# Kernel optimization log

Hardware: AMD Instinct MI355X
Metric: run time of the kernel (lower is better)

## Reference

```python
import jax, jax.numpy as jnp
import numpy as np

B, L, D, H, DFF = 8, 1024, 256, 8, 2048
DH = D // H


def setup_inputs() -> dict:
    key = jax.random.key(0)
    ks = jax.random.split(key, 12)

    def w(k, shape):
        return jax.random.normal(k, shape, dtype=jnp.float32) * 0.02

    # continuous padding: first `length` tokens valid, rest padded (mask True = pad)
    lengths = jax.random.randint(ks[0], (B,), L // 4, L + 1)
    mask = jnp.arange(L)[None, :] >= lengths[:, None]

    return {
        "src": jax.random.normal(ks[1], (B, L, D), dtype=jnp.float32),
        "src_key_padding_mask": mask,
        "in_proj_w": w(ks[2], (3 * D, D)),
        "in_proj_b": w(ks[3], (3 * D,)),
        "out_w": w(ks[4], (D, D)),
        "out_b": w(ks[5], (D,)),
        "proj_w": w(ks[6], (D, D)),
        "proj_b": w(ks[7], (D,)),
        "ff1_w": w(ks[8], (DFF, D)),
        "ff1_b": w(ks[9], (DFF,)),
        "ff2_w": w(ks[10], (D, DFF)),
        "ff2_b": w(ks[11], (D,)),
    }


def reference(src, src_key_padding_mask, in_proj_w, in_proj_b, out_w, out_b,
              proj_w, proj_b, ff1_w, ff1_b, ff2_w, ff2_b):
    mask = src_key_padding_mask  # [B, L], True = padding
    neg_inf = jnp.float32(-jnp.inf)

    # --- make_attn_mask (vectorized, continuous padding) ---
    s = (~mask).sum(axis=1).astype(jnp.float32)              # [B] valid lengths
    idx = jnp.arange(L, dtype=jnp.float32)
    dist = jnp.abs(idx[:, None] - idx[None, :])              # [L, L]
    valid_tok = idx[None, :] < s[:, None]                    # [B, L]
    pair_ok = valid_tok[:, :, None] & valid_tok[:, None, :]  # [B, L, L]
    bias = jnp.where(pair_ok, (s[:, None, None] - dist[None]) / s[:, None, None], neg_inf)
    # rows that are entirely -inf (padded query rows) are zeroed, like masked_fill
    row_pad = ~valid_tok                                     # [B, L]
    bias = jnp.where(row_pad[:, :, None], 0.0, bias)
    # key_padding_mask is merged additively (as in nn.MultiheadAttention)
    add_mask = bias + jnp.where(mask[:, None, :], neg_inf, 0.0)  # [B, L, L]

    # --- multi-head self-attention ---
    qkv = src @ in_proj_w.T + in_proj_b                      # [B, L, 3D]
    q, k, v = jnp.split(qkv, 3, axis=-1)

    def heads(t):
        return t.reshape(B, L, H, DH).transpose(0, 2, 1, 3)  # [B, H, L, DH]

    q, k, v = heads(q), heads(k), heads(v)
    scale = 1.0 / jnp.sqrt(jnp.float32(DH))
    scores = jnp.einsum('bhqd,bhkd->bhqk', q, k) * scale + add_mask[:, None]
    attn = jax.nn.softmax(scores, axis=-1)
    ctx = jnp.einsum('bhqk,bhkd->bhqd', attn, v)
    ctx = ctx.transpose(0, 2, 1, 3).reshape(B, L, D)
    h_attn = ctx @ out_w.T + out_b

    # --- residual proj + FFN (no layernorm, no dropout) ---
    h = src + (h_attn @ proj_w.T + proj_b)
    ff = jax.nn.gelu(h @ ff1_w.T + ff1_b, approximate=False) @ ff2_w.T + ff2_b
    h = h + ff

    # zero out padded rows (masked_fill with all_neg_inf)
    h = jnp.where(row_pad[:, :, None], 0.0, h)
    return h
```

## Files before the change

### kernel.cpp

```cpp
#include <hip/hip_runtime.h>
#include <hip/hip_bf16.h>


#define BB   8
#define LL   1024
#define DD   256
#define HHN  8
#define DHH  32
#define DFFN 2048

typedef __attribute__((ext_vector_type(8))) __bf16 bf16x8;
typedef __attribute__((ext_vector_type(4))) float f32x4;

__device__ inline void gload16(const void* g, void* l) {
  __builtin_amdgcn_global_load_lds(
      (const __attribute__((address_space(1))) void*)g,
      (__attribute__((address_space(3))) void*)l, 16, 0, 0);
}

__device__ inline bf16x8 cvt8(const float4 a, const float4 b) {
  bf16x8 o;
  o[0] = (__bf16)a.x; o[1] = (__bf16)a.y; o[2] = (__bf16)a.z; o[3] = (__bf16)a.w;
  o[4] = (__bf16)b.x; o[5] = (__bf16)b.y; o[6] = (__bf16)b.z; o[7] = (__bf16)b.w;
  return o;
}

#define NCVT2 (DFFN * DD)
#define NB_WC   128
#define NB_QKV  768
#define NB_CVT  512
#define BID_QKV  NB_WC
#define BID_CVT  (NB_WC + NB_QKV)
#define BID_LENS (BID_CVT + NB_CVT)
#define NB_TOTAL (BID_LENS + 1)

__global__ __launch_bounds__(256) void fused_pre_qkv(
    const float* __restrict__ src, const unsigned char* __restrict__ mb,
    const float* __restrict__ in_proj_w, const float* __restrict__ in_proj_b,
    const float* __restrict__ ff1_w, const float* __restrict__ ff2_w,
    const float* __restrict__ proj_w, const float* __restrict__ out_w,
    const float* __restrict__ proj_b, const float* __restrict__ out_b,
    __hip_bfloat16* __restrict__ qkv_bf, __hip_bfloat16* __restrict__ wff1_bf,
    __hip_bfloat16* __restrict__ wff2_bf, __hip_bfloat16* __restrict__ wc_bf,
    float* __restrict__ bc, int* __restrict__ lens) {
  __shared__ __bf16 As[2][64][32];
  __shared__ __bf16 Bs[2][128][32];
  __shared__ float red[256];
  __shared__ float pw[2][256];
  __shared__ int cnt8[BB];
  __shared__ int flag3f, flagNA;

  const int bid = blockIdx.x;
  const int tid = threadIdx.x;

  if (bid < NB_WC) {
    const int i0 = bid << 1;
    const int k = tid;
    pw[0][k] = proj_w[(size_t)i0 * DD + k];
    pw[1][k] = proj_w[(size_t)(i0 + 1) * DD + k];
    __syncthreads();
    float a0 = 0.f, a1 = 0.f;
#pragma unroll 8
    for (int n = 0; n < DD; ++n) {
      const float won = out_w[n * DD + k];
      a0 = fmaf(pw[0][n], won, a0);
      a1 = fmaf(pw[1][n], won, a1);
    }
    wc_bf[(size_t)i0 * DD + k] = (__hip_bfloat16)a0;
    wc_bf[(size_t)(i0 + 1) * DD + k] = (__hip_bfloat16)a1;
#pragma unroll
    for (int j = 0; j < 2; ++j) {
      red[k] = pw[j][k] * out_b[k];
      __syncthreads();
      for (int sft = 128; sft > 0; sft >>= 1) {
        if (k < sft) red[k] += red[k + sft];
        __syncthreads();
      }
      if (k == 0) bc[i0 + j] = proj_b[i0 + j] + red[0];
      __syncthreads();
    }
  } else if (bid < BID_CVT) {
    const int qb = bid - BID_QKV;
    const int x = qb % 6;
    const int y = qb / 6;
    const int c0 = x << 7;
    const int r0 = y << 6;
    const int w = tid >> 6;
    const int lane = tid & 63;
    const int c = lane & 15;
    const int hq = lane >> 4;
    const int h8 = hq << 3;
    const int wr = w >> 1, wc2 = w & 1;
    const int srow = tid >> 2;
    const int scol = (tid & 3) << 3;

    float4 ra[2], rb[2][2];
    auto LOADR = [&](int kt) {
      const int k0 = kt << 5;
      const float* ap = src + (size_t)(r0 + srow) * DD + k0 + scol;
      ra[0] = *(const float4*)ap;
      ra[1] = *(const float4*)(ap + 4);
#pragma unroll
      for (int ch = 0; ch < 2; ++ch) {
        const float* wp =
            in_proj_w + (size_t)(c0 + (ch << 6) + srow) * DD + k0 + scol;
        rb[ch][0] = *(const float4*)wp;
        rb[ch][1] = *(const float4*)(wp + 4);
      }
    };
    auto WRITEL = [&](int buf) {
      *(bf16x8*)&As[buf][srow][scol] = cvt8(ra[0], ra[1]);
#pragma unroll
      for (int ch = 0; ch < 2; ++ch)
        *(bf16x8*)&Bs[buf][(ch << 6) + srow][scol] = cvt8(rb[ch][0], rb[ch][1]);
    };

    f32x4 acc[2][4];
#pragma unroll
    for (int m = 0; m < 2; ++m)
#pragma unroll
      for (int n = 0; n < 4; ++n) acc[m][n] = (f32x4){0.f, 0.f, 0.f, 0.f};

    int buf = 0;
    LOADR(0);
    WRITEL(0);
    __syncthreads();
    for (int kt = 0; kt < 8; ++kt) {
      if (kt + 1 < 8) LOADR(kt + 1);
      bf16x8 af[2], bfr[4];
#pragma unroll
      for (int m = 0; m < 2; ++m)
        af[m] = *(const bf16x8*)&As[buf][wr * 32 + (m << 4) + c][h8];
#pragma unroll
      for (int n = 0; n < 4; ++n)
        bfr[n] = *(const bf16x8*)&Bs[buf][(wc2 << 6) + (n << 4) + c][h8];
#pragma unroll
      for (int m = 0; m < 2; ++m)
#pragma unroll
        for (int n = 0; n < 4; ++n)
          acc[m][n] = __builtin_amdgcn_mfma_f32_16x16x32_bf16(af[m], bfr[n],
                                                              acc[m][n], 0, 0, 0);
      if (kt + 1 < 8) WRITEL(buf ^ 1);
      __syncthreads();
      buf ^= 1;
    }

    float bv[4];
#pragma unroll
    for (int n = 0; n < 4; ++n)
      bv[n] = in_proj_b[c0 + (wc2 << 6) + (n << 4) + c];
#pragma unroll
    for (int m = 0; m < 2; ++m)
#pragma unroll
      for (int i = 0; i < 4; ++i) {
        const int gr = r0 + wr * 32 + (m << 4) + (hq << 2) + i;
#pragma unroll
        for (int n = 0; n < 4; ++n)
          qkv_bf[(size_t)gr * 768 + c0 + (wc2 << 6) + (n << 4) + c] =
              (__hip_bfloat16)(acc[m][n][i] + bv[n]);
      }
  } else if (bid < BID_LENS) {
    int i = (bid - BID_CVT) * 2048 + tid * 8;
    const float* s;
    __hip_bfloat16* d;
    if (i < NCVT2) { s = ff1_w; d = wff1_bf; }
    else { s = ff2_w; d = wff2_bf; i -= NCVT2; }
    const float4 a = *(const float4*)(s + i);
    const float4 b = *(const float4*)(s + i + 4);
    *(bf16x8*)(d + i) = cvt8(a, b);
  } else {
    if (tid == 0) { flag3f = 0; flagNA = 0; }
    if (tid < BB) cnt8[tid] = 0;
    __syncthreads();
    for (int i = tid; i < BB * LL; i += 256) {
      unsigned char v = mb[i];
      if (v) {
        if ((i & 3) == 3 && v == 0x3F) flag3f = 1;
        else if (i & 3) flagNA = 1;
      }
    }
    __syncthreads();
    const bool isfloat = (flag3f != 0);
    const bool isbool = (!isfloat) && (flagNA != 0);
    if (isbool) {
      for (int i = tid; i < BB * LL; i += 256)
        if (mb[i] == 0) atomicAdd(&cnt8[i >> 10], 1);
    } else {
      const int* mi = (const int*)mb;
      for (int i = tid; i < BB * LL; i += 256)
        if (mi[i] == 0) atomicAdd(&cnt8[i >> 10], 1);
    }
    __syncthreads();
    if (tid < BB) lens[tid] = cnt8[tid];
  }
}

template <int EPI, int BM, int BN>
__global__ __launch_bounds__(256) void gemm_bf16(
    const __hip_bfloat16* __restrict__ A, const __hip_bfloat16* __restrict__ W,
    const float* __restrict__ bias, const float* __restrict__ resid,
    float* __restrict__ Cf, __hip_bfloat16* __restrict__ Cb, const int M,
    const int N, const int K, const int* __restrict__ lens) {
  constexpr int MF = BM / 32;
  constexpr int NF = BN / 32;
  constexpr int CHA = BM / 64;
  constexpr int CHB = BN / 64;
  __shared__ __bf16 As[2][BM][32];
  __shared__ __bf16 Bs[2][BN][32];

  const int tid = threadIdx.x;
  const int w = tid >> 6;
  const int lane = tid & 63;
  const int c = lane & 15;
  const int hq = lane >> 4;
  const int h8 = hq << 3;
  const int wr = w >> 1, wc = w & 1;
  const int c0 = blockIdx.x * BN;
  const int r0 = blockIdx.y * BM;
  if ((r0 & (LL - 1)) >= lens[r0 >> 10]) return;

  const int srow = tid >> 2;
  const int scol = (tid & 3) << 3;

  auto STAGE = [&](int buf, int kt) {
    const int k0 = kt << 5;
#pragma unroll
    for (int ch = 0; ch < CHA; ++ch)
      gload16(A + (size_t)(r0 + (ch << 6) + srow) * K + k0 + scol,
              &As[buf][(ch << 6) + (w << 4)][0]);
#pragma unroll
    for (int ch = 0; ch < CHB; ++ch)
      gload16(W + (size_t)(c0 + (ch << 6) + srow) * K + k0 + scol,
              &Bs[buf][(ch << 6) + (w << 4)][0]);
  };

  f32x4 acc[MF][NF];
#pragma unroll
  for (int m = 0; m < MF; ++m)
#pragma unroll
    for (int n = 0; n < NF; ++n) acc[m][n] = (f32x4){0.f, 0.f, 0.f, 0.f};

  const int nkt = K >> 5;
  int buf = 0;
  STAGE(0, 0);
  __syncthreads();
  for (int kt = 0; kt < nkt; ++kt) {
    if (kt + 1 < nkt) STAGE(buf ^ 1, kt + 1);
    bf16x8 af[MF], bfr[NF];
#pragma unroll
    for (int m = 0; m < MF; ++m)
      af[m] = *(const bf16x8*)&As[buf][wr * (MF * 16) + (m << 4) + c][h8];
#pragma unroll
    for (int n = 0; n < NF; ++n)
      bfr[n] = *(const bf16x8*)&Bs[buf][wc * (NF * 16) + (n << 4) + c][h8];
#pragma unroll
    for (int m = 0; m < MF; ++m)
#pragma unroll
      for (int n = 0; n < NF; ++n)
        acc[m][n] =
            __builtin_amdgcn_mfma_f32_16x16x32_bf16(af[m], bfr[n], acc[m][n], 0, 0, 0);
    __syncthreads();
    buf ^= 1;
  }

  float bv[NF];
#pragma unroll
  for (int n = 0; n < NF; ++n) bv[n] = bias[c0 + wc * (NF * 16) + (n << 4) + c];

#pragma unroll
  for (int m = 0; m < MF; ++m) {
#pragma unroll
    for (int i = 0; i < 4; ++i) {
      const int gr = r0 + wr * (MF * 16) + (m << 4) + (hq << 2) + i;
#pragma unroll
      for (int n = 0; n < NF; ++n) {
        const int gc = c0 + wc * (NF * 16) + (n << 4) + c;
        float v = acc[m][n][i] + bv[n];
        if (EPI == 1) v = 0.5f * v * (1.0f + erff(v * 0.70710678118654752f));
        if (EPI == 2) {
          v += resid[(size_t)gr * N + gc];
          Cf[(size_t)gr * N + gc] = v;
        }
        Cb[(size_t)gr * N + gc] = (__hip_bfloat16)v;
      }
    }
  }
}

__global__ __launch_bounds__(256) void gemm_ff2_part(
    const __hip_bfloat16* __restrict__ A, const __hip_bfloat16* __restrict__ W,
    __hip_bfloat16* __restrict__ P, const int* __restrict__ lens) {
  __shared__ __bf16 As[2][64][32];
  __shared__ __bf16 Bs[2][128][32];

  const int tid = threadIdx.x;
  const int w = tid >> 6;
  const int lane = tid & 63;
  const int c = lane & 15;
  const int hq = lane >> 4;
  const int h8 = hq << 3;
  const int wr = w >> 1, wc = w & 1;
  const int c0 = blockIdx.x << 7;
  const int r0 = blockIdx.y << 6;
  if ((r0 & (LL - 1)) >= lens[r0 >> 10]) return;

  const int kz = blockIdx.z;
  const int kbase = kz << 9;
  const int srow = tid >> 2;
  const int scol = (tid & 3) << 3;

  auto STAGE = [&](int buf, int kt) {
    const int k0 = kbase + (kt << 5);
    gload16(A + (size_t)(r0 + srow) * DFFN + k0 + scol, &As[buf][w << 4][0]);
#pragma unroll
    for (int ch = 0; ch < 2; ++ch)
      gload16(W + (size_t)(c0 + (ch << 6) + srow) * DFFN + k0 + scol,
              &Bs[buf][(ch << 6) + (w << 4)][0]);
  };

  f32x4 acc[2][4];
#pragma unroll
  for (int m = 0; m < 2; ++m)
#pragma unroll
    for (int n = 0; n < 4; ++n) acc[m][n] = (f32x4){0.f, 0.f, 0.f, 0.f};

  int buf = 0;
  STAGE(0, 0);
  __syncthreads();
  for (int kt = 0; kt < 16; ++kt) {
    if (kt + 1 < 16) STAGE(buf ^ 1, kt + 1);
    bf16x8 af[2], bfr[4];
#pragma unroll
    for (int m = 0; m < 2; ++m)
      af[m] = *(const bf16x8*)&As[buf][wr * 32 + (m << 4) + c][h8];
#pragma unroll
    for (int n = 0; n < 4; ++n)
      bfr[n] = *(const bf16x8*)&Bs[buf][(wc << 6) + (n << 4) + c][h8];
#pragma unroll
    for (int m = 0; m < 2; ++m)
#pragma unroll
      for (int n = 0; n < 4; ++n)
        acc[m][n] =
            __builtin_amdgcn_mfma_f32_16x16x32_bf16(af[m], bfr[n], acc[m][n], 0, 0, 0);
    __syncthreads();
    buf ^= 1;
  }

  __hip_bfloat16* Pz = P + (size_t)kz * (BB * LL) * DD;
#pragma unroll
  for (int m = 0; m < 2; ++m)
#pragma unroll
    for (int i = 0; i < 4; ++i) {
      const int gr = r0 + wr * 32 + (m << 4) + (hq << 2) + i;
#pragma unroll
      for (int n = 0; n < 4; ++n)
        Pz[(size_t)gr * DD + c0 + (wc << 6) + (n << 4) + c] =
            (__hip_bfloat16)acc[m][n][i];
    }
}

__global__ __launch_bounds__(256) void ff2_reduce(
    const __hip_bfloat16* __restrict__ P, const float* __restrict__ resid,
    const float* __restrict__ bias, float* __restrict__ out,
    const int* __restrict__ lens) {
  const int idx = blockIdx.x * 256 + threadIdx.x;
  const int r = idx >> 6;
  const int c4 = (idx & 63) << 2;
  float4 o;
  if ((r & (LL - 1)) >= lens[r >> 10]) {
    o.x = o.y = o.z = o.w = 0.f;
  } else {
    const size_t base = (size_t)r * DD + c4;
    o = *(const float4*)&resid[base];
    const float4 bv = *(const float4*)&bias[c4];
    o.x += bv.x; o.y += bv.y; o.z += bv.z; o.w += bv.w;
#pragma unroll
    for (int z = 0; z < 4; ++z) {
      const ushort4 pu = *(const ushort4*)(P + (size_t)z * (BB * LL) * DD + base);
      o.x += __bfloat162float(*(const __hip_bfloat16*)&pu.x);
      o.y += __bfloat162float(*(const __hip_bfloat16*)&pu.y);
      o.z += __bfloat162float(*(const __hip_bfloat16*)&pu.z);
      o.w += __bfloat162float(*(const __hip_bfloat16*)&pu.w);
    }
  }
  *(float4*)&out[(size_t)r * DD + c4] = o;
}

__global__ __launch_bounds__(256) void attn_fwd_mfma(
    const __hip_bfloat16* __restrict__ qkv, __hip_bfloat16* __restrict__ ctx,
    const int* __restrict__ lens) {
  __shared__ __bf16 Ks[2][64][56];
  __shared__ __bf16 Vt[2][32][66];
  __shared__ __bf16 Pl[4][16][72];

  const int tid = threadIdx.x;
  const int q0 = blockIdx.x << 6;
  const int hh = blockIdx.y;
  const int b = blockIdx.z;
  const int slen = lens[b];
  if (q0 >= slen) return;

  const int w = tid >> 6;
  const int lane = tid & 63;
  const int c = lane & 15;
  const int h = lane >> 4;
  const int h8 = h << 3;

  const float L2E = 1.44269504f;
  const float sf = (float)slen;
  const float cb = -7.0f * L2E;
  const float cd = (1.0f / sf) * L2E;
  const float qscale = 0.17677669529663689f * L2E;

  bf16x8 qf;
  {
    const int qrow = q0 + (w << 4) + c;
    const bf16x8 qraw =
        *(const bf16x8*)(qkv + (size_t)(b * LL + qrow) * 768 + hh * DHH + h8);
#pragma unroll
    for (int j = 0; j < 8; ++j) qf[j] = (__bf16)((float)qraw[j] * qscale);
  }

  f32x4 acc0 = {0.f, 0.f, 0.f, 0.f};
  f32x4 acc1 = {0.f, 0.f, 0.f, 0.f};
  float lsum[4] = {0.f, 0.f, 0.f, 0.f};

  const int skey = tid >> 2;
  const int sdg = (tid & 3) << 3;
  const int ntk = (slen + 63) >> 6;
  const int qg = q0 + (w << 4) + (h << 2);

  const __hip_bfloat16* kvbase = qkv + (size_t)b * LL * 768 + 256 + hh * DHH + sdg;

  bf16x8 kreg, vreg;
  {
    const __hip_bfloat16* kb = kvbase + (size_t)skey * 768;
    kreg = *(const bf16x8*)kb;
    vreg = *(const bf16x8*)(kb + 256);
    *(bf16x8*)&Ks[0][skey][sdg] = kreg;
#pragma unroll
    for (int j = 0; j < 8; ++j) Vt[0][sdg + j][skey] = vreg[j];
  }
  if (ntk > 1) {
    const __hip_bfloat16* kb = kvbase + (size_t)(64 + skey) * 768;
    kreg = *(const bf16x8*)kb;
    vreg = *(const bf16x8*)(kb + 256);
  }
  __syncthreads();

  for (int kt = 0; kt < ntk; ++kt) {
    const int p = kt & 1;
    const int kbase = kt << 6;

    f32x4 st[4];
    __builtin_amdgcn_s_setprio(1);
#pragma unroll
    for (int t = 0; t < 4; ++t) {
      const bf16x8 kf = *(const bf16x8*)&Ks[p][(t << 4) + c][h8];
      st[t] = __builtin_amdgcn_mfma_f32_16x16x32_bf16(
          qf, kf, (f32x4){0.f, 0.f, 0.f, 0.f}, 0, 0, 0);
    }
    __builtin_amdgcn_s_setprio(0);

    if (kbase + 64 <= slen) {
#pragma unroll
      for (int t = 0; t < 4; ++t) {
        const float kjf = (float)(kbase + (t << 4) + c);
#pragma unroll
        for (int i = 0; i < 4; ++i) {
          const float dist = fabsf((float)(qg + i) - kjf);
          const float pv = __builtin_amdgcn_exp2f(st[t][i] + cb - dist * cd);
          lsum[i] += pv;
          Pl[w][(h << 2) + i][c + (t << 4)] = (__bf16)pv;
        }
      }
    } else {
#pragma unroll
      for (int t = 0; t < 4; ++t) {
        const int kj = kbase + (t << 4) + c;
        const bool kvalid = kj < slen;
        const float kjf = (float)kj;
#pragma unroll
        for (int i = 0; i < 4; ++i) {
          const float dist = fabsf((float)(qg + i) - kjf);
          const float arg = kvalid ? (st[t][i] + cb - dist * cd) : -1e30f;
          const float pv = __builtin_amdgcn_exp2f(arg);
          lsum[i] += pv;
          Pl[w][(h << 2) + i][c + (t << 4)] = (__bf16)pv;
        }
      }
    }

    asm volatile("s_waitcnt lgkmcnt(0)" ::: "memory");

    __builtin_amdgcn_s_setprio(1);
#pragma unroll
    for (int n = 0; n < 2; ++n) {
      const bf16x8 pf = *(const bf16x8*)&Pl[w][c][h8 + (n << 5)];
      const uint32_t* v0p = (const uint32_t*)&Vt[p][c][h8 + (n << 5)];
      const uint32_t* v1p = (const uint32_t*)&Vt[p][16 + c][h8 + (n << 5)];
      union { uint32_t u[4]; bf16x8 v; } t0, t1;
#pragma unroll
      for (int j = 0; j < 4; ++j) { t0.u[j] = v0p[j]; t1.u[j] = v1p[j]; }
      acc0 = __builtin_amdgcn_mfma_f32_16x16x32_bf16(pf, t0.v, acc0, 0, 0, 0);
      acc1 = __builtin_amdgcn_mfma_f32_16x16x32_bf16(pf, t1.v, acc1, 0, 0, 0);
    }
    __builtin_amdgcn_s_setprio(0);

    if (kt + 1 < ntk) {
      *(bf16x8*)&Ks[p ^ 1][skey][sdg] = kreg;
#pragma unroll
      for (int j = 0; j < 8; ++j) Vt[p ^ 1][sdg + j][skey] = vreg[j];
      if (kt + 2 < ntk) {
        const __hip_bfloat16* kb = kvbase + (size_t)(((kt + 2) << 6) + skey) * 768;
        kreg = *(const bf16x8*)kb;
        vreg = *(const bf16x8*)(kb + 256);
      }
    }
    __syncthreads();
  }

#pragma unroll
  for (int i = 0; i < 4; ++i) {
    float l = lsum[i];
    l += __shfl_xor(l, 1);
    l += __shfl_xor(l, 2);
    l += __shfl_xor(l, 4);
    l += __shfl_xor(l, 8);
    const float il = 1.0f / l;
    __hip_bfloat16* op =
        ctx + (size_t)(b * LL + q0 + (w << 4) + (h << 2) + i) * 256 + hh * DHH;
    op[c] = (__hip_bfloat16)(acc0[i] * il);
    op[c + 16] = (__hip_bfloat16)(acc1[i] * il);
  }
}

extern "C" void kernel_launch(void* const* d_in, const int* in_sizes, int n_in,
                              void* d_out, int out_size, void* d_ws,
                              size_t ws_size, hipStream_t stream) {
  (void)in_sizes; (void)n_in; (void)out_size; (void)ws_size;
  const float* src = (const float*)d_in[0];
  const unsigned char* mask = (const unsigned char*)d_in[1];
  const float* in_proj_w = (const float*)d_in[2];
  const float* in_proj_b = (const float*)d_in[3];
  const float* out_w = (const float*)d_in[4];
  const float* out_b = (const float*)d_in[5];
  const float* proj_w = (const float*)d_in[6];
  const float* proj_b = (const float*)d_in[7];
  const float* ff1_w = (const float*)d_in[8];
  const float* ff1_b = (const float*)d_in[9];
  const float* ff2_w = (const float*)d_in[10];
  const float* ff2_b = (const float*)d_in[11];
  float* out = (float*)d_out;

  const int M = BB * LL;
  char* p = (char*)d_ws;
  __hip_bfloat16* qkv_bf = (__hip_bfloat16*)p; p += (size_t)M * 768 * 2;
  __hip_bfloat16* ctx_bf = (__hip_bfloat16*)p; p += (size_t)M * 256 * 2;
  float* hbuf_f = (float*)p;                    p += (size_t)M * 256 * 4;
  __hip_bfloat16* hbuf_bf = (__hip_bfloat16*)p; p += (size_t)M * 256 * 2;
  __hip_bfloat16* ff1o_bf = (__hip_bfloat16*)p; p += (size_t)M * 2048 * 2;
  __hip_bfloat16* wff1_bf = (__hip_bfloat16*)p; p += (size_t)2048 * 256 * 2;
  __hip_bfloat16* wff2_bf = (__hip_bfloat16*)p; p += (size_t)256 * 2048 * 2;
  __hip_bfloat16* wc_bf = (__hip_bfloat16*)p;   p += (size_t)256 * 256 * 2;
  float* bc = (float*)p;                        p += 256 * 4;
  int* lens = (int*)p;                          p += 256;
  __hip_bfloat16* pbuf = (__hip_bfloat16*)p;    p += (size_t)4 * M * 256 * 2;

  fused_pre_qkv<<<NB_TOTAL, 256, 0, stream>>>(
      src, mask, in_proj_w, in_proj_b, ff1_w, ff2_w, proj_w, out_w, proj_b,
      out_b, qkv_bf, wff1_bf, wff2_bf, wc_bf, bc, lens);

  attn_fwd_mfma<<<dim3(LL / 64, HHN, BB), 256, 0, stream>>>(qkv_bf, ctx_bf, lens);

  gemm_bf16<2, 64, 64><<<dim3(4, 128), 256, 0, stream>>>(
      ctx_bf, wc_bf, bc, src, hbuf_f, hbuf_bf, M, 256, 256, lens);

  gemm_bf16<1, 128, 128><<<dim3(16, 64), 256, 0, stream>>>(
      hbuf_bf, wff1_bf, ff1_b, nullptr, nullptr, ff1o_bf, M, 2048, 256, lens);

  gemm_ff2_part<<<dim3(2, 128, 4), 256, 0, stream>>>(ff1o_bf, wff2_bf, pbuf, lens);

  ff2_reduce<<<M * 256 / 4 / 256, 256, 0, stream>>>(pbuf, hbuf_f, ff2_b, out, lens);
}
```

Before: 114.2 us.

## Replace GEMMs with small-tile full-K-slab kernel and drop FF2 split-K reduction

```diff
diff --git a/kernel.cpp b/kernel.cpp
--- a/kernel.cpp
+++ b/kernel.cpp
@@ -11,12 +11,6 @@
 
 typedef __attribute__((ext_vector_type(8))) __bf16 bf16x8;
 typedef __attribute__((ext_vector_type(4))) float f32x4;
-
-__device__ inline void gload16(const void* g, void* l) {
-  __builtin_amdgcn_global_load_lds(
-      (const __attribute__((address_space(1))) void*)g,
-      (__attribute__((address_space(3))) void*)l, 16, 0, 0);
-}
 
 __device__ inline bf16x8 cvt8(const float4 a, const float4 b) {
   bf16x8 o;
@@ -195,18 +189,14 @@
   }
 }
 
-template <int EPI, int BM, int BN>
-__global__ __launch_bounds__(256) void gemm_bf16(
+template <int EPI, int NIT>
+__global__ __launch_bounds__(256) void gemm_os(
     const __hip_bfloat16* __restrict__ A, const __hip_bfloat16* __restrict__ W,
     const float* __restrict__ bias, const float* __restrict__ resid,
-    float* __restrict__ Cf, __hip_bfloat16* __restrict__ Cb, const int M,
-    const int N, const int K, const int* __restrict__ lens) {
-  constexpr int MF = BM / 32;
-  constexpr int NF = BN / 32;
-  constexpr int CHA = BM / 64;
-  constexpr int CHB = BN / 64;
-  __shared__ __bf16 As[2][BM][32];
-  __shared__ __bf16 Bs[2][BN][32];
+    float* __restrict__ Cf, __hip_bfloat16* __restrict__ Cb, const int N,
+    const int* __restrict__ lens) {
+  __shared__ __bf16 Al[32][264];
+  __shared__ __bf16 Bl[64][264];
 
   const int tid = threadIdx.x;
   const int w = tid >> 6;
@@ -215,175 +205,83 @@
   const int hq = lane >> 4;
   const int h8 = hq << 3;
   const int wr = w >> 1, wc = w & 1;
-  const int c0 = blockIdx.x * BN;
-  const int r0 = blockIdx.y * BM;
-  if ((r0 & (LL - 1)) >= lens[r0 >> 10]) return;
-
-  const int srow = tid >> 2;
-  const int scol = (tid & 3) << 3;
-
-  auto STAGE = [&](int buf, int kt) {
-    const int k0 = kt << 5;
-#pragma unroll
-    for (int ch = 0; ch < CHA; ++ch)
-      gload16(A + (size_t)(r0 + (ch << 6) + srow) * K + k0 + scol,
-              &As[buf][(ch << 6) + (w << 4)][0]);
-#pragma unroll
-    for (int ch = 0; ch < CHB; ++ch)
-      gload16(W + (size_t)(c0 + (ch << 6) + srow) * K + k0 + scol,
-              &Bs[buf][(ch << 6) + (w << 4)][0]);
+  const int c0 = blockIdx.x << 6;
+  const int r0 = blockIdx.y << 5;
+  const int K = NIT * 256;
+  const int mylen = lens[r0 >> 10];
+
+  if ((r0 & (LL - 1)) >= mylen) {
+    if (EPI == 3) {
+      const int rr = tid >> 3;
+      const int cc = (tid & 7) << 3;
+      const float4 z = {0.f, 0.f, 0.f, 0.f};
+      *(float4*)&Cf[(size_t)(r0 + rr) * N + c0 + cc] = z;
+      *(float4*)&Cf[(size_t)(r0 + rr) * N + c0 + cc + 4] = z;
+    }
+    return;
+  }
+
+  const int ar = tid >> 3, asg = (tid & 7) << 5;
+  const int br = tid >> 2, bsg = (tid & 3) << 6;
+
+  bf16x8 ra[4], rb[8];
+  auto LOADR = [&](int t) {
+    const __hip_bfloat16* ap = A + (size_t)(r0 + ar) * K + t * 256 + asg;
+#pragma unroll
+    for (int j = 0; j < 4; ++j) ra[j] = *(const bf16x8*)(ap + j * 8);
+    const __hip_bfloat16* bp = W + (size_t)(c0 + br) * K + t * 256 + bsg;
+#pragma unroll
+    for (int j = 0; j < 8; ++j) rb[j] = *(const bf16x8*)(bp + j * 8);
   };
-
-  f32x4 acc[MF][NF];
-#pragma unroll
-  for (int m = 0; m < MF; ++m)
-#pragma unroll
-    for (int n = 0; n < NF; ++n) acc[m][n] = (f32x4){0.f, 0.f, 0.f, 0.f};
-
-  const int nkt = K >> 5;
-  int buf = 0;
-  STAGE(0, 0);
+  auto WRITEL = [&]() {
+#pragma unroll
+    for (int j = 0; j < 4; ++j) *(bf16x8*)&Al[ar][asg + j * 8] = ra[j];
+#pragma unroll
+    for (int j = 0; j < 8; ++j) *(bf16x8*)&Bl[br][bsg + j * 8] = rb[j];
+  };
+
+  f32x4 acc[2] = {{0.f, 0.f, 0.f, 0.f}, {0.f, 0.f, 0.f, 0.f}};
+
+  LOADR(0);
+  WRITEL();
   __syncthreads();
-  for (int kt = 0; kt < nkt; ++kt) {
-    if (kt + 1 < nkt) STAGE(buf ^ 1, kt + 1);
-    bf16x8 af[MF], bfr[NF];
-#pragma unroll
-    for (int m = 0; m < MF; ++m)
-      af[m] = *(const bf16x8*)&As[buf][wr * (MF * 16) + (m << 4) + c][h8];
-#pragma unroll
-    for (int n = 0; n < NF; ++n)
-      bfr[n] = *(const bf16x8*)&Bs[buf][wc * (NF * 16) + (n << 4) + c][h8];
-#pragma unroll
-    for (int m = 0; m < MF; ++m)
-#pragma unroll
-      for (int n = 0; n < NF; ++n)
-        acc[m][n] =
-            __builtin_amdgcn_mfma_f32_16x16x32_bf16(af[m], bfr[n], acc[m][n], 0, 0, 0);
-    __syncthreads();
-    buf ^= 1;
-  }
-
-  float bv[NF];
-#pragma unroll
-  for (int n = 0; n < NF; ++n) bv[n] = bias[c0 + wc * (NF * 16) + (n << 4) + c];
-
-#pragma unroll
-  for (int m = 0; m < MF; ++m) {
-#pragma unroll
-    for (int i = 0; i < 4; ++i) {
-      const int gr = r0 + wr * (MF * 16) + (m << 4) + (hq << 2) + i;
-#pragma unroll
-      for (int n = 0; n < NF; ++n) {
-        const int gc = c0 + wc * (NF * 16) + (n << 4) + c;
-        float v = acc[m][n][i] + bv[n];
-        if (EPI == 1) v = 0.5f * v * (1.0f + erff(v * 0.70710678118654752f));
-        if (EPI == 2) {
-          v += resid[(size_t)gr * N + gc];
-          Cf[(size_t)gr * N + gc] = v;
-        }
-        Cb[(size_t)gr * N + gc] = (__hip_bfloat16)v;
-      }
-    }
-  }
-}
-
-__global__ __launch_bounds__(256) void gemm_ff2_part(
-    const __hip_bfloat16* __restrict__ A, const __hip_bfloat16* __restrict__ W,
-    __hip_bfloat16* __restrict__ P, const int* __restrict__ lens) {
-  __shared__ __bf16 As[2][64][32];
-  __shared__ __bf16 Bs[2][128][32];
-
-  const int tid = threadIdx.x;
-  const int w = tid >> 6;
-  const int lane = tid & 63;
-  const int c = lane & 15;
-  const int hq = lane >> 4;
-  const int h8 = hq << 3;
-  const int wr = w >> 1, wc = w & 1;
-  const int c0 = blockIdx.x << 7;
-  const int r0 = blockIdx.y << 6;
-  if ((r0 & (LL - 1)) >= lens[r0 >> 10]) return;
-
-  const int kz = blockIdx.z;
-  const int kbase = kz << 9;
-  const int srow = tid >> 2;
-  const int scol = (tid & 3) << 3;
-
-  auto STAGE = [&](int buf, int kt) {
-    const int k0 = kbase + (kt << 5);
-    gload16(A + (size_t)(r0 + srow) * DFFN + k0 + scol, &As[buf][w << 4][0]);
-#pragma unroll
-    for (int ch = 0; ch < 2; ++ch)
-      gload16(W + (size_t)(c0 + (ch << 6) + srow) * DFFN + k0 + scol,
-              &Bs[buf][(ch << 6) + (w << 4)][0]);
-  };
-
-  f32x4 acc[2][4];
-#pragma unroll
-  for (int m = 0; m < 2; ++m)
-#pragma unroll
-    for (int n = 0; n < 4; ++n) acc[m][n] = (f32x4){0.f, 0.f, 0.f, 0.f};
-
-  int buf = 0;
-  STAGE(0, 0);
-  __syncthreads();
-  for (int kt = 0; kt < 16; ++kt) {
-    if (kt + 1 < 16) STAGE(buf ^ 1, kt + 1);
-    bf16x8 af[2], bfr[4];
-#pragma unroll
-    for (int m = 0; m < 2; ++m)
-      af[m] = *(const bf16x8*)&As[buf][wr * 32 + (m << 4) + c][h8];
-#pragma unroll
-    for (int n = 0; n < 4; ++n)
-      bfr[n] = *(const bf16x8*)&Bs[buf][(wc << 6) + (n << 4) + c][h8];
-#pragma unroll
-    for (int m = 0; m < 2; ++m)
-#pragma unroll
-      for (int n = 0; n < 4; ++n)
-        acc[m][n] =
-            __builtin_amdgcn_mfma_f32_16x16x32_bf16(af[m], bfr[n], acc[m][n], 0, 0, 0);
-    __syncthreads();
-    buf ^= 1;
-  }
-
-  __hip_bfloat16* Pz = P + (size_t)kz * (BB * LL) * DD;
-#pragma unroll
-  for (int m = 0; m < 2; ++m)
-#pragma unroll
-    for (int i = 0; i < 4; ++i) {
-      const int gr = r0 + wr * 32 + (m << 4) + (hq << 2) + i;
-#pragma unroll
-      for (int n = 0; n < 4; ++n)
-        Pz[(size_t)gr * DD + c0 + (wc << 6) + (n << 4) + c] =
-            (__hip_bfloat16)acc[m][n][i];
-    }
-}
-
-__global__ __launch_bounds__(256) void ff2_reduce(
-    const __hip_bfloat16* __restrict__ P, const float* __restrict__ resid,
-    const float* __restrict__ bias, float* __restrict__ out,
-    const int* __restrict__ lens) {
-  const int idx = blockIdx.x * 256 + threadIdx.x;
-  const int r = idx >> 6;
-  const int c4 = (idx & 63) << 2;
-  float4 o;
-  if ((r & (LL - 1)) >= lens[r >> 10]) {
-    o.x = o.y = o.z = o.w = 0.f;
-  } else {
-    const size_t base = (size_t)r * DD + c4;
-    o = *(const float4*)&resid[base];
-    const float4 bv = *(const float4*)&bias[c4];
-    o.x += bv.x; o.y += bv.y; o.z += bv.z; o.w += bv.w;
-#pragma unroll
-    for (int z = 0; z < 4; ++z) {
-      const ushort4 pu = *(const ushort4*)(P + (size_t)z * (BB * LL) * DD + base);
-      o.x += __bfloat162float(*(const __hip_bfloat16*)&pu.x);
-      o.y += __bfloat162float(*(const __hip_bfloat16*)&pu.y);
-      o.z += __bfloat162float(*(const __hip_bfloat16*)&pu.z);
-      o.w += __bfloat162float(*(const __hip_bfloat16*)&pu.w);
-    }
-  }
-  *(float4*)&out[(size_t)r * DD + c4] = o;
+  for (int t = 0; t < NIT; ++t) {
+    if (t + 1 < NIT) LOADR(t + 1);
+#pragma unroll
+    for (int k0 = 0; k0 < 8; ++k0) {
+      const bf16x8 af = *(const bf16x8*)&Al[wr * 16 + c][k0 * 32 + h8];
+#pragma unroll
+      for (int n = 0; n < 2; ++n) {
+        const bf16x8 bf = *(const bf16x8*)&Bl[wc * 32 + (n << 4) + c][k0 * 32 + h8];
+        acc[n] = __builtin_amdgcn_mfma_f32_16x16x32_bf16(af, bf, acc[n], 0, 0, 0);
+      }
+    }
+    if (t + 1 < NIT) {
+      __syncthreads();
+      WRITEL();
+      __syncthreads();
+    }
+  }
+
+  float bv[2];
+#pragma unroll
+  for (int n = 0; n < 2; ++n) bv[n] = bias[c0 + wc * 32 + (n << 4) + c];
+
+#pragma unroll
+  for (int i = 0; i < 4; ++i) {
+    const int gr = r0 + wr * 16 + (hq << 2) + i;
+    const bool zrow = (EPI == 3) && ((gr & (LL - 1)) >= mylen);
+#pragma unroll
+    for (int n = 0; n < 2; ++n) {
+      const int gc = c0 + wc * 32 + (n << 4) + c;
+      float v = acc[n][i] + bv[n];
+      if (EPI == 1) v = 0.5f * v * (1.0f + erff(v * 0.70710678118654752f));
+      if (EPI >= 2) v += resid[(size_t)gr * N + gc];
+      if (EPI == 3 && zrow) v = 0.f;
+      if (EPI >= 2) Cf[(size_t)gr * N + gc] = v;
+      if (EPI != 3) Cb[(size_t)gr * N + gc] = (__hip_bfloat16)v;
+    }
+  }
 }
 
 __global__ __launch_bounds__(256) void attn_fwd_mfma(
@@ -565,7 +463,6 @@
   __hip_bfloat16* wc_bf = (__hip_bfloat16*)p;   p += (size_t)256 * 256 * 2;
   float* bc = (float*)p;                        p += 256 * 4;
   int* lens = (int*)p;                          p += 256;
-  __hip_bfloat16* pbuf = (__hip_bfloat16*)p;    p += (size_t)4 * M * 256 * 2;
 
   fused_pre_qkv<<<NB_TOTAL, 256, 0, stream>>>(
       src, mask, in_proj_w, in_proj_b, ff1_w, ff2_w, proj_w, out_w, proj_b,
@@ -573,13 +470,12 @@
 
   attn_fwd_mfma<<<dim3(LL / 64, HHN, BB), 256, 0, stream>>>(qkv_bf, ctx_bf, lens);
 
-  gemm_bf16<2, 64, 64><<<dim3(4, 128), 256, 0, stream>>>(
-      ctx_bf, wc_bf, bc, src, hbuf_f, hbuf_bf, M, 256, 256, lens);
-
-  gemm_bf16<1, 128, 128><<<dim3(16, 64), 256, 0, stream>>>(
-      hbuf_bf, wff1_bf, ff1_b, nullptr, nullptr, ff1o_bf, M, 2048, 256, lens);
-
-  gemm_ff2_part<<<dim3(2, 128, 4), 256, 0, stream>>>(ff1o_bf, wff2_bf, pbuf, lens);
-
-  ff2_reduce<<<M * 256 / 4 / 256, 256, 0, stream>>>(pbuf, hbuf_f, ff2_b, out, lens);
+  gemm_os<2, 1><<<dim3(4, 256), 256, 0, stream>>>(
+      ctx_bf, wc_bf, bc, src, hbuf_f, hbuf_bf, DD, lens);
+
+  gemm_os<1, 1><<<dim3(32, 256), 256, 0, stream>>>(
+      hbuf_bf, wff1_bf, ff1_b, nullptr, nullptr, ff1o_bf, DFFN, lens);
+
+  gemm_os<3, 8><<<dim3(4, 256), 256, 0, stream>>>(
+      ff1o_bf, wff2_bf, ff2_b, hbuf_f, out, nullptr, DD, lens);
 }
```

Result: slower. 149.3 us (+30.7%).

## Replace split-K FF2 GEMM and reduce kernel with single fused-epilogue GEMM

Applied to the files above, without the earlier changes.

```diff
diff --git a/kernel.cpp b/kernel.cpp
--- a/kernel.cpp
+++ b/kernel.cpp
@@ -217,7 +217,22 @@
   const int wr = w >> 1, wc = w & 1;
   const int c0 = blockIdx.x * BN;
   const int r0 = blockIdx.y * BM;
-  if ((r0 & (LL - 1)) >= lens[r0 >> 10]) return;
+  const int mylen = lens[r0 >> 10];
+
+  if ((r0 & (LL - 1)) >= mylen) {
+    if (EPI == 3) {
+      constexpr int NF4 = BM * BN / 4 / 256;
+#pragma unroll
+      for (int k = 0; k < NF4; ++k) {
+        const int f4 = k * 256 + tid;
+        const int rr = f4 / (BN / 4);
+        const int cc = (f4 % (BN / 4)) << 2;
+        *(float4*)&Cf[(size_t)(r0 + rr) * N + c0 + cc] =
+            (float4){0.f, 0.f, 0.f, 0.f};
+      }
+    }
+    return;
+  }
 
   const int srow = tid >> 2;
   const int scol = (tid & 3) << 3;
@@ -272,118 +287,19 @@
 #pragma unroll
     for (int i = 0; i < 4; ++i) {
       const int gr = r0 + wr * (MF * 16) + (m << 4) + (hq << 2) + i;
+      const bool zrow = (EPI == 3) && ((gr & (LL - 1)) >= mylen);
 #pragma unroll
       for (int n = 0; n < NF; ++n) {
         const int gc = c0 + wc * (NF * 16) + (n << 4) + c;
         float v = acc[m][n][i] + bv[n];
         if (EPI == 1) v = 0.5f * v * (1.0f + erff(v * 0.70710678118654752f));
-        if (EPI == 2) {
-          v += resid[(size_t)gr * N + gc];
-          Cf[(size_t)gr * N + gc] = v;
-        }
-        Cb[(size_t)gr * N + gc] = (__hip_bfloat16)v;
-      }
-    }
-  }
-}
-
-__global__ __launch_bounds__(256) void gemm_ff2_part(
-    const __hip_bfloat16* __restrict__ A, const __hip_bfloat16* __restrict__ W,
-    __hip_bfloat16* __restrict__ P, const int* __restrict__ lens) {
-  __shared__ __bf16 As[2][64][32];
-  __shared__ __bf16 Bs[2][128][32];
-
-  const int tid = threadIdx.x;
-  const int w = tid >> 6;
-  const int lane = tid & 63;
-  const int c = lane & 15;
-  const int hq = lane >> 4;
-  const int h8 = hq << 3;
-  const int wr = w >> 1, wc = w & 1;
-  const int c0 = blockIdx.x << 7;
-  const int r0 = blockIdx.y << 6;
-  if ((r0 & (LL - 1)) >= lens[r0 >> 10]) return;
-
-  const int kz = blockIdx.z;
-  const int kbase = kz << 9;
-  const int srow = tid >> 2;
-  const int scol = (tid & 3) << 3;
-
-  auto STAGE = [&](int buf, int kt) {
-    const int k0 = kbase + (kt << 5);
-    gload16(A + (size_t)(r0 + srow) * DFFN + k0 + scol, &As[buf][w << 4][0]);
-#pragma unroll
-    for (int ch = 0; ch < 2; ++ch)
-      gload16(W + (size_t)(c0 + (ch << 6) + srow) * DFFN + k0 + scol,
-              &Bs[buf][(ch << 6) + (w << 4)][0]);
-  };
-
-  f32x4 acc[2][4];
-#pragma unroll
-  for (int m = 0; m < 2; ++m)
-#pragma unroll
-    for (int n = 0; n < 4; ++n) acc[m][n] = (f32x4){0.f, 0.f, 0.f, 0.f};
-
-  int buf = 0;
-  STAGE(0, 0);
-  __syncthreads();
-  for (int kt = 0; kt < 16; ++kt) {
-    if (kt + 1 < 16) STAGE(buf ^ 1, kt + 1);
-    bf16x8 af[2], bfr[4];
-#pragma unroll
-    for (int m = 0; m < 2; ++m)
-      af[m] = *(const bf16x8*)&As[buf][wr * 32 + (m << 4) + c][h8];
-#pragma unroll
-    for (int n = 0; n < 4; ++n)
-      bfr[n] = *(const bf16x8*)&Bs[buf][(wc << 6) + (n << 4) + c][h8];
-#pragma unroll
-    for (int m = 0; m < 2; ++m)
-#pragma unroll
-      for (int n = 0; n < 4; ++n)
-        acc[m][n] =
-            __builtin_amdgcn_mfma_f32_16x16x32_bf16(af[m], bfr[n], acc[m][n], 0, 0, 0);
-    __syncthreads();
-    buf ^= 1;
-  }
-
-  __hip_bfloat16* Pz = P + (size_t)kz * (BB * LL) * DD;
-#pragma unroll
-  for (int m = 0; m < 2; ++m)
-#pragma unroll
-    for (int i = 0; i < 4; ++i) {
-      const int gr = r0 + wr * 32 + (m << 4) + (hq << 2) + i;
-#pragma unroll
-      for (int n = 0; n < 4; ++n)
-        Pz[(size_t)gr * DD + c0 + (wc << 6) + (n << 4) + c] =
-            (__hip_bfloat16)acc[m][n][i];
-    }
-}
-
-__global__ __launch_bounds__(256) void ff2_reduce(
-    const __hip_bfloat16* __restrict__ P, const float* __restrict__ resid,
-    const float* __restrict__ bias, float* __restrict__ out,
-    const int* __restrict__ lens) {
-  const int idx = blockIdx.x * 256 + threadIdx.x;
-  const int r = idx >> 6;
-  const int c4 = (idx & 63) << 2;
-  float4 o;
-  if ((r & (LL - 1)) >= lens[r >> 10]) {
-    o.x = o.y = o.z = o.w = 0.f;
-  } else {
-    const size_t base = (size_t)r * DD + c4;
-    o = *(const float4*)&resid[base];
-    const float4 bv = *(const float4*)&bias[c4];
-    o.x += bv.x; o.y += bv.y; o.z += bv.z; o.w += bv.w;
-#pragma unroll
-    for (int z = 0; z < 4; ++z) {
-      const ushort4 pu = *(const ushort4*)(P + (size_t)z * (BB * LL) * DD + base);
-      o.x += __bfloat162float(*(const __hip_bfloat16*)&pu.x);
-      o.y += __bfloat162float(*(const __hip_bfloat16*)&pu.y);
-      o.z += __bfloat162float(*(const __hip_bfloat16*)&pu.z);
-      o.w += __bfloat162float(*(const __hip_bfloat16*)&pu.w);
-    }
-  }
-  *(float4*)&out[(size_t)r * DD + c4] = o;
+        if (EPI >= 2) v += resid[(size_t)gr * N + gc];
+        if (EPI == 3 && zrow) v = 0.f;
+        if (EPI >= 2) Cf[(size_t)gr * N + gc] = v;
+        if (EPI != 3) Cb[(size_t)gr * N + gc] = (__hip_bfloat16)v;
+      }
+    }
+  }
 }
 
 __global__ __launch_bounds__(256) void attn_fwd_mfma(
@@ -565,7 +481,6 @@
   __hip_bfloat16* wc_bf = (__hip_bfloat16*)p;   p += (size_t)256 * 256 * 2;
   float* bc = (float*)p;                        p += 256 * 4;
   int* lens = (int*)p;                          p += 256;
-  __hip_bfloat16* pbuf = (__hip_bfloat16*)p;    p += (size_t)4 * M * 256 * 2;
 
   fused_pre_qkv<<<NB_TOTAL, 256, 0, stream>>>(
       src, mask, in_proj_w, in_proj_b, ff1_w, ff2_w, proj_w, out_w, proj_b,
@@ -579,7 +494,6 @@
   gemm_bf16<1, 128, 128><<<dim3(16, 64), 256, 0, stream>>>(
       hbuf_bf, wff1_bf, ff1_b, nullptr, nullptr, ff1o_bf, M, 2048, 256, lens);
 
-  gemm_ff2_part<<<dim3(2, 128, 4), 256, 0, stream>>>(ff1o_bf, wff2_bf, pbuf, lens);
-
-  ff2_reduce<<<M * 256 / 4 / 256, 256, 0, stream>>>(pbuf, hbuf_f, ff2_b, out, lens);
-}
+  gemm_bf16<3, 64, 64><<<dim3(4, 128), 256, 0, stream>>>(
+      ff1o_bf, wff2_bf, ff2_b, hbuf_f, out, nullptr, M, 256, 2048, lens);
+}
```

Measured after the change: 117.6 us. 1.03x slower.

## Move FF weight bf16 conversions into later GEMM kernels as extra blocks

Applied to the files above, without the earlier changes.

```diff
diff --git a/kernel.cpp b/kernel.cpp
--- a/kernel.cpp
+++ b/kernel.cpp
@@ -25,23 +25,26 @@
   return o;
 }
 
-#define NCVT2 (DFFN * DD)
+__device__ inline void cvt_block(const float* __restrict__ s,
+                                 __hip_bfloat16* __restrict__ d, int i0) {
+  const int i = i0 + threadIdx.x * 8;
+  const float4 a = *(const float4*)(s + i);
+  const float4 b = *(const float4*)(s + i + 4);
+  *(bf16x8*)(d + i) = cvt8(a, b);
+}
+
 #define NB_WC   128
 #define NB_QKV  768
-#define NB_CVT  512
 #define BID_QKV  NB_WC
-#define BID_CVT  (NB_WC + NB_QKV)
-#define BID_LENS (BID_CVT + NB_CVT)
-#define NB_TOTAL (BID_LENS + 1)
+#define BID_LENS (NB_WC + NB_QKV)
+#define NB_K1    (BID_LENS + 1)
 
 __global__ __launch_bounds__(256) void fused_pre_qkv(
     const float* __restrict__ src, const unsigned char* __restrict__ mb,
     const float* __restrict__ in_proj_w, const float* __restrict__ in_proj_b,
-    const float* __restrict__ ff1_w, const float* __restrict__ ff2_w,
     const float* __restrict__ proj_w, const float* __restrict__ out_w,
     const float* __restrict__ proj_b, const float* __restrict__ out_b,
-    __hip_bfloat16* __restrict__ qkv_bf, __hip_bfloat16* __restrict__ wff1_bf,
-    __hip_bfloat16* __restrict__ wff2_bf, __hip_bfloat16* __restrict__ wc_bf,
+    __hip_bfloat16* __restrict__ qkv_bf, __hip_bfloat16* __restrict__ wc_bf,
     float* __restrict__ bc, int* __restrict__ lens) {
   __shared__ __bf16 As[2][64][32];
   __shared__ __bf16 Bs[2][128][32];
@@ -79,7 +82,7 @@
       if (k == 0) bc[i0 + j] = proj_b[i0 + j] + red[0];
       __syncthreads();
     }
-  } else if (bid < BID_CVT) {
+  } else if (bid < BID_LENS) {
     const int qb = bid - BID_QKV;
     const int x = qb % 6;
     const int y = qb / 6;
@@ -159,15 +162,6 @@
           qkv_bf[(size_t)gr * 768 + c0 + (wc2 << 6) + (n << 4) + c] =
               (__hip_bfloat16)(acc[m][n][i] + bv[n]);
       }
-  } else if (bid < BID_LENS) {
-    int i = (bid - BID_CVT) * 2048 + tid * 8;
-    const float* s;
-    __hip_bfloat16* d;
-    if (i < NCVT2) { s = ff1_w; d = wff1_bf; }
-    else { s = ff2_w; d = wff2_bf; i -= NCVT2; }
-    const float4 a = *(const float4*)(s + i);
-    const float4 b = *(const float4*)(s + i + 4);
-    *(bf16x8*)(d + i) = cvt8(a, b);
   } else {
     if (tid == 0) { flag3f = 0; flagNA = 0; }
     if (tid < BB) cnt8[tid] = 0;
@@ -196,11 +190,11 @@
 }
 
 template <int EPI, int BM, int BN>
-__global__ __launch_bounds__(256) void gemm_bf16(
+__device__ __forceinline__ void gemm_body(
     const __hip_bfloat16* __restrict__ A, const __hip_bfloat16* __restrict__ W,
     const float* __restrict__ bias, const float* __restrict__ resid,
-    float* __restrict__ Cf, __hip_bfloat16* __restrict__ Cb, const int M,
-    const int N, const int K, const int* __restrict__ lens) {
+    float* __restrict__ Cf, __hip_bfloat16* __restrict__ Cb, const int N,
+    const int K, const int* __restrict__ lens, const int bx, const int by) {
   constexpr int MF = BM / 32;
   constexpr int NF = BN / 32;
   constexpr int CHA = BM / 64;
@@ -215,8 +209,8 @@
   const int hq = lane >> 4;
   const int h8 = hq << 3;
   const int wr = w >> 1, wc = w & 1;
-  const int c0 = blockIdx.x * BN;
-  const int r0 = blockIdx.y * BM;
+  const int c0 = bx * BN;
+  const int r0 = by * BM;
   if ((r0 & (LL - 1)) >= lens[r0 >> 10]) return;
 
   const int srow = tid >> 2;
@@ -284,6 +278,35 @@
         Cb[(size_t)gr * N + gc] = (__hip_bfloat16)v;
       }
     }
+  }
+}
+
+__global__ __launch_bounds__(256) void proj_cvt(
+    const __hip_bfloat16* __restrict__ ctx, const __hip_bfloat16* __restrict__ wc,
+    const float* __restrict__ bc, const float* __restrict__ src,
+    float* __restrict__ hbuf_f, __hip_bfloat16* __restrict__ hbuf_bf,
+    const int* __restrict__ lens, const float* __restrict__ ff1_w,
+    __hip_bfloat16* __restrict__ wff1_bf) {
+  const int bid = blockIdx.x;
+  if (bid < 512) {
+    gemm_body<2, 64, 64>(ctx, wc, bc, src, hbuf_f, hbuf_bf, DD, DD, lens,
+                         bid & 3, bid >> 2);
+  } else {
+    cvt_block(ff1_w, wff1_bf, (bid - 512) * 2048);
+  }
+}
+
+__global__ __launch_bounds__(256) void ff1_cvt(
+    const __hip_bfloat16* __restrict__ hbuf_bf,
+    const __hip_bfloat16* __restrict__ wff1_bf, const float* __restrict__ ff1_b,
+    __hip_bfloat16* __restrict__ ff1o_bf, const int* __restrict__ lens,
+    const float* __restrict__ ff2_w, __hip_bfloat16* __restrict__ wff2_bf) {
+  const int bid = blockIdx.x;
+  if (bid < 1024) {
+    gemm_body<1, 128, 128>(hbuf_bf, wff1_bf, ff1_b, nullptr, nullptr, ff1o_bf,
+                           DFFN, DD, lens, bid & 15, bid >> 4);
+  } else {
+    cvt_block(ff2_w, wff2_bf, (bid - 1024) * 2048);
   }
 }
 
@@ -567,17 +590,17 @@
   int* lens = (int*)p;                          p += 256;
   __hip_bfloat16* pbuf = (__hip_bfloat16*)p;    p += (size_t)4 * M * 256 * 2;
 
-  fused_pre_qkv<<<NB_TOTAL, 256, 0, stream>>>(
-      src, mask, in_proj_w, in_proj_b, ff1_w, ff2_w, proj_w, out_w, proj_b,
-      out_b, qkv_bf, wff1_bf, wff2_bf, wc_bf, bc, lens);
+  fused_pre_qkv<<<NB_K1, 256, 0, stream>>>(src, mask, in_proj_w, in_proj_b,
+                                           proj_w, out_w, proj_b, out_b,
+                                           qkv_bf, wc_bf, bc, lens);
 
   attn_fwd_mfma<<<dim3(LL / 64, HHN, BB), 256, 0, stream>>>(qkv_bf, ctx_bf, lens);
 
-  gemm_bf16<2, 64, 64><<<dim3(4, 128), 256, 0, stream>>>(
-      ctx_bf, wc_bf, bc, src, hbuf_f, hbuf_bf, M, 256, 256, lens);
-
-  gemm_bf16<1, 128, 128><<<dim3(16, 64), 256, 0, stream>>>(
-      hbuf_bf, wff1_bf, ff1_b, nullptr, nullptr, ff1o_bf, M, 2048, 256, lens);
+  proj_cvt<<<768, 256, 0, stream>>>(ctx_bf, wc_bf, bc, src, hbuf_f, hbuf_bf,
+                                    lens, ff1_w, wff1_bf);
+
+  ff1_cvt<<<1280, 256, 0, stream>>>(hbuf_bf, wff1_bf, ff1_b, ff1o_bf, lens,
+                                    ff2_w, wff2_bf);
 
   gemm_ff2_part<<<dim3(2, 128, 4), 256, 0, stream>>>(ff1o_bf, wff2_bf, pbuf, lens);
 
```

Result: no change. 115.6 us (+1.2%).
